# Kernel tuning notes

Measured on AMD Instinct MI355X. Metric: run time of the kernel, lower is better.

Reference implementation:

```python
import jax, jax.numpy as jnp
import numpy as np

B = 65536
N_CHILDREN = 512
HIDDEN = 64


def setup_inputs() -> dict:
    key = jax.random.key(0)
    k1, k2, k3, k4, k5, k6, k7 = jax.random.split(key, 7)
    x_cpm = jax.random.normal(k1, (B, N_CHILDREN), dtype=jnp.float32)
    x_cons = jax.random.normal(k2, (B, 1), dtype=jnp.float32)
    # per-child capacities, strictly positive (used as divisor)
    cap = jax.random.uniform(k3, (1, N_CHILDREN), dtype=jnp.float32) + 0.5
    # small MLP params (torch Linear layout: W is (out, in))
    s1 = 1.0 / np.sqrt(N_CHILDREN + 1)
    s2 = 1.0 / np.sqrt(HIDDEN)
    W1 = jax.random.normal(k4, (HIDDEN, N_CHILDREN + 1), dtype=jnp.float32) * s1
    b1 = jax.random.normal(k5, (HIDDEN,), dtype=jnp.float32) * s1
    W2 = jax.random.normal(k6, (N_CHILDREN, HIDDEN), dtype=jnp.float32) * s2
    b2 = jax.random.normal(k7, (N_CHILDREN,), dtype=jnp.float32) * s2
    return {"x_cpm": x_cpm, "x_cons": x_cons, "cap": cap,
            "W1": W1, "b1": b1, "W2": W2, "b2": b2}


def reference(x_cpm, x_cons, cap, W1, b1, W2, b2):
    cap_sum = jnp.sum(cap)  # scalar Cap_sum
    # epsilon: (B, 1) residual of the aggregate constraint
    epsilon = (x_cons * cap_sum - jnp.sum(x_cpm * cap, axis=1, keepdims=True)) / cap_sum
    concat_input = jnp.concatenate([x_cpm, epsilon], axis=1)  # (B, n_l + 1)
    h1 = jax.nn.relu(concat_input @ W1.T + b1)                # (B, 64)
    z = h1 @ W2.T + b2                                        # (B, n_l)
    # symmetric activation: tanh then row-normalize by the signed sum
    signed = jnp.tanh(z)
    h = signed / jnp.sum(signed, axis=1, keepdims=True)
    # reconcile
    x_c = (x_cpm * cap + h * epsilon * cap_sum) / cap
    return x_c
```

## Files before the change

### kernel.cpp

```cpp
#include <hip/hip_runtime.h>
#include <hip/hip_fp16.h>
#include <math.h>

#define THREADS 256
#define RPB 32
#define NBLK (65536 / RPB)

#define WS_W1    0
#define WS_W1_CH 3072
#define WS_W2    (16 * WS_W1_CH)
#define WS_W2_CH 8192
#define WS_W1L   (WS_W2 + 4 * WS_W2_CH)

#define OFF_W    0
#define SZ_W     32768
#define W1BUF_B  12288
#define OFF_H1   (OFF_W + SZ_W)
#define SZ_H1    (RPB * 68 * 4)
#define OFF_CI   (OFF_H1 + SZ_H1)
#define SZ_CI    2048
#define OFF_EPS  (OFF_CI + SZ_CI)
#define OFF_EPSC (OFF_EPS + 128)
#define SMEM_BYTES (OFF_EPSC + 128)

__device__ __forceinline__ float fast_tanh(float z) {
    float e = __expf(2.0f * z);
    return fmaf(-2.0f, __builtin_amdgcn_rcpf(e + 1.0f), 1.0f);
}

__global__ __launch_bounds__(256) void prep_kernel(
    const float* __restrict__ W1, const float* __restrict__ W2,
    float* __restrict__ ws)
{
    int tid = blockIdx.x * 256 + threadIdx.x;
    {
        int it = tid >> 11;
        int rem = tid & 2047;
        int jj = rem >> 6, c = rem & 63;
        ws[WS_W1 + it * WS_W1_CH + jj * 68 + c] = W1[c * 513 + it * 32 + jj];
    }
    {
        int j = tid & 3, kf4 = (tid >> 2) & 15, n = (tid >> 6) & 127, ch = tid >> 13;
        int swz = kf4 ^ ((9 * (n >> 2) + (n & 3)) & 15);
        ws[WS_W2 + ch * WS_W2_CH + n * 64 + swz * 4 + j] = W2[tid];
    }
    if (tid < 64) ws[WS_W1L + tid] = W1[tid * 513 + 512];
}

__global__ __launch_bounds__(THREADS, 3) void fused_rgu(
    const float* __restrict__ x, const float* __restrict__ xcons,
    const float* __restrict__ cap, const float* __restrict__ b1,
    const float* __restrict__ b2, const float* __restrict__ ws,
    float* __restrict__ out)
{
    extern __shared__ __align__(16) char smem[];
    float*          s_w    = (float*)(smem + OFF_W);
    float*          s_h1   = (float*)(smem + OFF_H1);
    float*          s_ci   = (float*)(smem + OFF_CI);
    float*          s_eps  = (float*)(smem + OFF_EPS);
    float*          s_epsC = (float*)(smem + OFF_EPSC);

    const int t    = threadIdx.x;
    const int lane = t & 63;
    const int wv   = t >> 6;
    const long r0  = (long)blockIdx.x * RPB;

    {
        const float4* src = (const float4*)(ws + WS_W1);
        float4* dst = (float4*)(smem + OFF_W);
        dst[t] = src[t]; dst[t + 256] = src[t + 256]; dst[t + 512] = src[t + 512];
    }

    float4 capA = *(const float4*)(cap + 4 * lane);
    float4 capB = *(const float4*)(cap + 256 + 4 * lane);
    {
        float c0 = cap[t], c1 = cap[t + 256];
        s_ci[t] = 1.0f / c0; s_ci[t + 256] = 1.0f / c1;
    }
    float capSum;
    {
        float p = capA.x + capA.y + capA.z + capA.w
                + capB.x + capB.y + capB.z + capB.w;
        #pragma unroll
        for (int m = 1; m < 64; m <<= 1) p += __shfl_xor(p, m, 64);
        capSum = p;
    }
    const float invCapSum = 1.0f / capSum;

    #pragma unroll
    for (int rr = 0; rr < 8; ++rr) {
        int r = wv * 8 + rr;
        const float* xr = x + (r0 + r) * 512;
        float4 xA = *(const float4*)(xr + 4 * lane);
        float4 xB = *(const float4*)(xr + 256 + 4 * lane);
        float d = fmaf(xA.x, capA.x, fmaf(xA.y, capA.y,
                  fmaf(xA.z, capA.z, fmaf(xA.w, capA.w,
                  fmaf(xB.x, capB.x, fmaf(xB.y, capB.y,
                  fmaf(xB.z, capB.z, xB.w * capB.w)))))));
        #pragma unroll
        for (int m = 1; m < 64; m <<= 1) d += __shfl_xor(d, m, 64);
        if (lane == 0) {
            float epsC = fmaf(xcons[r0 + r], capSum, -d);
            s_epsC[r] = epsC;
            s_eps[r]  = epsC * invCapSum;
        }
    }
    __syncthreads();

    const int rg = t >> 4;
    const int cg = t & 15;
    float acc0[4] = {0.f, 0.f, 0.f, 0.f};
    float acc1[4] = {0.f, 0.f, 0.f, 0.f};
    {
        const float* xg0 = x + (r0 + 2 * rg) * 512;
        const float* xg1 = xg0 + 512;
        for (int it = 0; it < 16; ++it) {
            const int b = it & 1;
            if (it < 15) {
                const float4* src = (const float4*)(ws + WS_W1 + (it + 1) * WS_W1_CH);
                float4* dst = (float4*)(smem + OFF_W + (b ^ 1) * W1BUF_B);
                dst[t] = src[t]; dst[t + 256] = src[t + 256]; dst[t + 512] = src[t + 512];
            }
            const float* w = (const float*)(smem + OFF_W + b * W1BUF_B);
            const int k0 = it * 32;
            #pragma unroll
            for (int j4 = 0; j4 < 8; ++j4) {
                float4 xv0 = *(const float4*)(xg0 + k0 + j4 * 4);
                float4 xv1 = *(const float4*)(xg1 + k0 + j4 * 4);
                const float* wb = &w[(j4 * 4) * 68 + 4 * cg];
                float wr[4][4];
                #pragma unroll
                for (int dj = 0; dj < 4; ++dj) {
                    float4 w4 = *(const float4*)(wb + dj * 68);
                    wr[dj][0] = w4.x; wr[dj][1] = w4.y; wr[dj][2] = w4.z; wr[dj][3] = w4.w;
                }
                #pragma unroll
                for (int m = 0; m < 4; ++m) {
                    acc0[m] = fmaf(xv0.x, wr[0][m], fmaf(xv0.y, wr[1][m],
                              fmaf(xv0.z, wr[2][m], fmaf(xv0.w, wr[3][m], acc0[m]))));
                    acc1[m] = fmaf(xv1.x, wr[0][m], fmaf(xv1.y, wr[1][m],
                              fmaf(xv1.z, wr[2][m], fmaf(xv1.w, wr[3][m], acc1[m]))));
                }
            }
            __syncthreads();
        }
        float4 b1v = *(const float4*)(b1 + 4 * cg);
        float4 wl  = *(const float4*)(ws + WS_W1L + 4 * cg);
        #pragma unroll
        for (int i = 0; i < 2; ++i) {
            float e = s_eps[2 * rg + i];
            const float* a = i ? acc1 : acc0;
            float4 h;
            h.x = fmaxf(a[0] + fmaf(e, wl.x, b1v.x), 0.f);
            h.y = fmaxf(a[1] + fmaf(e, wl.y, b1v.y), 0.f);
            h.z = fmaxf(a[2] + fmaf(e, wl.z, b1v.z), 0.f);
            h.w = fmaxf(a[3] + fmaf(e, wl.w, b1v.w), 0.f);
            *(float4*)&s_h1[(2 * rg + i) * 68 + 4 * cg] = h;
        }
    }

    const int ng  = t & 31;
    const int rg2 = t >> 5;
    float rsum[4] = {0.f, 0.f, 0.f, 0.f};
    unsigned tp[4][4][2];
    #pragma unroll
    for (int ch = 0; ch < 4; ++ch) {
        __syncthreads();
        {
            const float4* src = (const float4*)(ws + WS_W2 + ch * WS_W2_CH);
            float4* dst = (float4*)(smem + OFF_W);
            #pragma unroll
            for (int e8 = 0; e8 < 8; ++e8) dst[e8 * 256 + t] = src[e8 * 256 + t];
        }
        __syncthreads();
        const int n0 = ch * 128;
        float4 b2v = *(const float4*)(b2 + n0 + 4 * ng);
        float za[4][4];
        #pragma unroll
        for (int i = 0; i < 4; ++i) {
            za[i][0] = b2v.x; za[i][1] = b2v.y; za[i][2] = b2v.z; za[i][3] = b2v.w;
        }
        #pragma unroll
        for (int kf4 = 0; kf4 < 16; ++kf4) {
            float hr[4][4];
            #pragma unroll
            for (int i = 0; i < 4; ++i) {
                float4 h = *(const float4*)&s_h1[(rg2 * 4 + i) * 68 + kf4 * 4];
                hr[i][0] = h.x; hr[i][1] = h.y; hr[i][2] = h.z; hr[i][3] = h.w;
            }
            float wr2[4][4];
            #pragma unroll
            for (int m = 0; m < 4; ++m) {
                int nl = 4 * ng + m;
                int swz = kf4 ^ ((9 * ng + m) & 15);
                float4 w = *(const float4*)&s_w[nl * 64 + swz * 4];
                wr2[m][0] = w.x; wr2[m][1] = w.y; wr2[m][2] = w.z; wr2[m][3] = w.w;
            }
            #pragma unroll
            for (int i = 0; i < 4; ++i)
                #pragma unroll
                for (int m = 0; m < 4; ++m)
                    za[i][m] = fmaf(hr[i][0], wr2[m][0], fmaf(hr[i][1], wr2[m][1],
                               fmaf(hr[i][2], wr2[m][2], fmaf(hr[i][3], wr2[m][3], za[i][m]))));
        }
        #pragma unroll
        for (int i = 0; i < 4; ++i) {
            float t0 = fast_tanh(za[i][0]);
            float t1 = fast_tanh(za[i][1]);
            float t2 = fast_tanh(za[i][2]);
            float t3 = fast_tanh(za[i][3]);
            rsum[i] += (t0 + t1) + (t2 + t3);
            __half2 h01 = __floats2half2_rn(t0, t1);
            __half2 h23 = __floats2half2_rn(t2, t3);
            tp[ch][i][0] = *(unsigned*)&h01;
            tp[ch][i][1] = *(unsigned*)&h23;
        }
    }

    float rs[4];
    #pragma unroll
    for (int i = 0; i < 4; ++i) {
        float s = rsum[i];
        #pragma unroll
        for (int msk = 1; msk < 32; msk <<= 1) s += __shfl_xor(s, msk, 64);
        rs[i] = s_epsC[rg2 * 4 + i] / s;
    }

    #pragma unroll
    for (int ch = 0; ch < 4; ++ch) {
        const int c = ch * 128 + 4 * ng;
        float4 ci = *(const float4*)&s_ci[c];
        #pragma unroll
        for (int i = 0; i < 4; ++i) {
            const int r = rg2 * 4 + i;
            float4 xv = *(const float4*)(x + (r0 + r) * 512 + c);
            __half2 h01 = *(__half2*)&tp[ch][i][0];
            __half2 h23 = *(__half2*)&tp[ch][i][1];
            float2 f01 = __half22float2(h01);
            float2 f23 = __half22float2(h23);
            float ri = rs[i];
            float4 o;
            o.x = fmaf(f01.x, ri * ci.x, xv.x);
            o.y = fmaf(f01.y, ri * ci.y, xv.y);
            o.z = fmaf(f23.x, ri * ci.z, xv.z);
            o.w = fmaf(f23.y, ri * ci.w, xv.w);
            *(float4*)(out + (r0 + r) * 512 + c) = o;
        }
    }
}

extern "C" void kernel_launch(void* const* d_in, const int* in_sizes, int n_in,
                              void* d_out, int out_size, void* d_ws, size_t ws_size,
                              hipStream_t stream) {
    const float* x     = (const float*)d_in[0];
    const float* xcons = (const float*)d_in[1];
    const float* cap   = (const float*)d_in[2];
    const float* W1    = (const float*)d_in[3];
    const float* b1    = (const float*)d_in[4];
    const float* W2    = (const float*)d_in[5];
    const float* b2    = (const float*)d_in[6];
    float* out         = (float*)d_out;
    float* ws          = (float*)d_ws;

    (void)in_sizes; (void)n_in; (void)out_size; (void)ws_size;

    prep_kernel<<<128, 256, 0, stream>>>(W1, W2, ws);

    hipFuncSetAttribute((const void*)fused_rgu,
                        hipFuncAttributeMaxDynamicSharedMemorySize, SMEM_BYTES);
    fused_rgu<<<NBLK, THREADS, SMEM_BYTES, stream>>>(
        x, xcons, cap, b1, b2, ws, out);
}
```

Measured before the change: 389.3 us.

## Shrink shared-memory footprint and W2 tiles to raise occupancy to five blocks

Drops the W1 chunk padding from 3072 to 2304 floats and splits W2 into eight 64-output chunks instead of four 128-output chunks, which cuts the shared weight buffer from 32 KB to about 17 KB. The second GEMM now reuses the first GEMM's 2-row by 4-column thread mapping, and b2 is staged in shared memory. Launch bounds go from 3 to 5 blocks per SM to hide more global-memory latency. In exchange there are more W2 chunk loads and barriers, less register reuse per thread (2 rows instead of 4), and a tighter register budget.

```diff
diff --git a/kernel.cpp b/kernel.cpp
--- a/kernel.cpp
+++ b/kernel.cpp
@@ -7,19 +7,21 @@
 #define NBLK (65536 / RPB)
 
 #define WS_W1    0
-#define WS_W1_CH 3072
+#define WS_W1_CH 2304
 #define WS_W2    (16 * WS_W1_CH)
-#define WS_W2_CH 8192
-#define WS_W1L   (WS_W2 + 4 * WS_W2_CH)
+#define WS_W2_CH 4096
+#define WS_W1L   (WS_W2 + 8 * WS_W2_CH)
 
 #define OFF_W    0
-#define SZ_W     32768
-#define W1BUF_B  12288
+#define W1BUF_B  8704
+#define SZ_W     17408
 #define OFF_H1   (OFF_W + SZ_W)
 #define SZ_H1    (RPB * 68 * 4)
 #define OFF_CI   (OFF_H1 + SZ_H1)
 #define SZ_CI    2048
-#define OFF_EPS  (OFF_CI + SZ_CI)
+#define OFF_B2   (OFF_CI + SZ_CI)
+#define SZ_B2    2048
+#define OFF_EPS  (OFF_B2 + SZ_B2)
 #define OFF_EPSC (OFF_EPS + 128)
 #define SMEM_BYTES (OFF_EPSC + 128)
 
@@ -40,14 +42,14 @@
         ws[WS_W1 + it * WS_W1_CH + jj * 68 + c] = W1[c * 513 + it * 32 + jj];
     }
     {
-        int j = tid & 3, kf4 = (tid >> 2) & 15, n = (tid >> 6) & 127, ch = tid >> 13;
+        int j = tid & 3, kf4 = (tid >> 2) & 15, n = (tid >> 6) & 63, ch = tid >> 12;
         int swz = kf4 ^ ((9 * (n >> 2) + (n & 3)) & 15);
         ws[WS_W2 + ch * WS_W2_CH + n * 64 + swz * 4 + j] = W2[tid];
     }
     if (tid < 64) ws[WS_W1L + tid] = W1[tid * 513 + 512];
 }
 
-__global__ __launch_bounds__(THREADS, 3) void fused_rgu(
+__global__ __launch_bounds__(THREADS, 5) void fused_rgu(
     const float* __restrict__ x, const float* __restrict__ xcons,
     const float* __restrict__ cap, const float* __restrict__ b1,
     const float* __restrict__ b2, const float* __restrict__ ws,
@@ -57,6 +59,7 @@
     float*          s_w    = (float*)(smem + OFF_W);
     float*          s_h1   = (float*)(smem + OFF_H1);
     float*          s_ci   = (float*)(smem + OFF_CI);
+    float*          s_b2   = (float*)(smem + OFF_B2);
     float*          s_eps  = (float*)(smem + OFF_EPS);
     float*          s_epsC = (float*)(smem + OFF_EPSC);
 
@@ -68,7 +71,8 @@
     {
         const float4* src = (const float4*)(ws + WS_W1);
         float4* dst = (float4*)(smem + OFF_W);
-        dst[t] = src[t]; dst[t + 256] = src[t + 256]; dst[t + 512] = src[t + 512];
+        dst[t] = src[t]; dst[t + 256] = src[t + 256];
+        if (t < 32) dst[t + 512] = src[t + 512];
     }
 
     float4 capA = *(const float4*)(cap + 4 * lane);
@@ -76,6 +80,7 @@
     {
         float c0 = cap[t], c1 = cap[t + 256];
         s_ci[t] = 1.0f / c0; s_ci[t + 256] = 1.0f / c1;
+        s_b2[t] = b2[t];     s_b2[t + 256] = b2[t + 256];
     }
     float capSum;
     {
@@ -119,7 +124,8 @@
             if (it < 15) {
                 const float4* src = (const float4*)(ws + WS_W1 + (it + 1) * WS_W1_CH);
                 float4* dst = (float4*)(smem + OFF_W + (b ^ 1) * W1BUF_B);
-                dst[t] = src[t]; dst[t + 256] = src[t + 256]; dst[t + 512] = src[t + 512];
+                dst[t] = src[t]; dst[t + 256] = src[t + 256];
+                if (t < 32) dst[t + 512] = src[t + 512];
             }
             const float* w = (const float*)(smem + OFF_W + b * W1BUF_B);
             const int k0 = it * 32;
@@ -159,52 +165,50 @@
         }
     }
 
-    const int ng  = t & 31;
-    const int rg2 = t >> 5;
-    float rsum[4] = {0.f, 0.f, 0.f, 0.f};
-    unsigned tp[4][4][2];
-    #pragma unroll
-    for (int ch = 0; ch < 4; ++ch) {
+    float rsum[2] = {0.f, 0.f};
+    unsigned tp[8][2][2];
+    #pragma unroll
+    for (int ch = 0; ch < 8; ++ch) {
         __syncthreads();
         {
             const float4* src = (const float4*)(ws + WS_W2 + ch * WS_W2_CH);
             float4* dst = (float4*)(smem + OFF_W);
             #pragma unroll
-            for (int e8 = 0; e8 < 8; ++e8) dst[e8 * 256 + t] = src[e8 * 256 + t];
+            for (int e4 = 0; e4 < 4; ++e4) dst[e4 * 256 + t] = src[e4 * 256 + t];
         }
         __syncthreads();
-        const int n0 = ch * 128;
-        float4 b2v = *(const float4*)(b2 + n0 + 4 * ng);
-        float za[4][4];
-        #pragma unroll
-        for (int i = 0; i < 4; ++i) {
+        const int n0 = ch * 64;
+        float4 b2v = *(const float4*)&s_b2[n0 + 4 * cg];
+        float za[2][4];
+        #pragma unroll
+        for (int i = 0; i < 2; ++i) {
             za[i][0] = b2v.x; za[i][1] = b2v.y; za[i][2] = b2v.z; za[i][3] = b2v.w;
         }
         #pragma unroll
         for (int kf4 = 0; kf4 < 16; ++kf4) {
-            float hr[4][4];
-            #pragma unroll
-            for (int i = 0; i < 4; ++i) {
-                float4 h = *(const float4*)&s_h1[(rg2 * 4 + i) * 68 + kf4 * 4];
+            float hr[2][4];
+            #pragma unroll
+            for (int i = 0; i < 2; ++i) {
+                float4 h = *(const float4*)&s_h1[(2 * rg + i) * 68 + kf4 * 4];
                 hr[i][0] = h.x; hr[i][1] = h.y; hr[i][2] = h.z; hr[i][3] = h.w;
             }
             float wr2[4][4];
             #pragma unroll
             for (int m = 0; m < 4; ++m) {
-                int nl = 4 * ng + m;
-                int swz = kf4 ^ ((9 * ng + m) & 15);
+                int nl = 4 * cg + m;
+                int swz = kf4 ^ ((9 * cg + m) & 15);
                 float4 w = *(const float4*)&s_w[nl * 64 + swz * 4];
                 wr2[m][0] = w.x; wr2[m][1] = w.y; wr2[m][2] = w.z; wr2[m][3] = w.w;
             }
             #pragma unroll
-            for (int i = 0; i < 4; ++i)
+            for (int i = 0; i < 2; ++i)
                 #pragma unroll
                 for (int m = 0; m < 4; ++m)
                     za[i][m] = fmaf(hr[i][0], wr2[m][0], fmaf(hr[i][1], wr2[m][1],
                                fmaf(hr[i][2], wr2[m][2], fmaf(hr[i][3], wr2[m][3], za[i][m]))));
         }
         #pragma unroll
-        for (int i = 0; i < 4; ++i) {
+        for (int i = 0; i < 2; ++i) {
             float t0 = fast_tanh(za[i][0]);
             float t1 = fast_tanh(za[i][1]);
             float t2 = fast_tanh(za[i][2]);
@@ -217,22 +221,22 @@
         }
     }
 
-    float rs[4];
-    #pragma unroll
-    for (int i = 0; i < 4; ++i) {
+    float rs[2];
+    #pragma unroll
+    for (int i = 0; i < 2; ++i) {
         float s = rsum[i];
         #pragma unroll
-        for (int msk = 1; msk < 32; msk <<= 1) s += __shfl_xor(s, msk, 64);
-        rs[i] = s_epsC[rg2 * 4 + i] / s;
-    }
-
-    #pragma unroll
-    for (int ch = 0; ch < 4; ++ch) {
-        const int c = ch * 128 + 4 * ng;
+        for (int msk = 1; msk < 16; msk <<= 1) s += __shfl_xor(s, msk, 64);
+        rs[i] = s_epsC[2 * rg + i] / s;
+    }
+
+    #pragma unroll
+    for (int ch = 0; ch < 8; ++ch) {
+        const int c = ch * 64 + 4 * cg;
         float4 ci = *(const float4*)&s_ci[c];
         #pragma unroll
-        for (int i = 0; i < 4; ++i) {
-            const int r = rg2 * 4 + i;
+        for (int i = 0; i < 2; ++i) {
+            const int r = 2 * rg + i;
             float4 xv = *(const float4*)(x + (r0 + r) * 512 + c);
             __half2 h01 = *(__half2*)&tp[ch][i][0];
             __half2 h23 = *(__half2*)&tp[ch][i][1];
```

After: 509.3 us. 30.8% more time.

## Retile first GEMM to 4 rows x 2 cols per thread with swizzled packed W1

Applied to the files above, without the earlier changes.

Changes the first-layer GEMM mapping from 2 rows x 4 hidden units per thread to 4 rows x 2 hidden units. W1 is repacked in the prep kernel into an XOR-swizzled, pair-interleaved layout without padding, so each W1 stage is smaller and loads as two float4s per k-group. The aim is fewer LDS reads per FMA and a smaller staging buffer, but each thread now issues more global x loads per step. b2 is staged in shared memory, and launch bounds drop from 3 to 2 blocks per CU, which gives the compiler more registers at the cost of occupancy.

```diff
diff --git a/kernel.cpp b/kernel.cpp
--- a/kernel.cpp
+++ b/kernel.cpp
@@ -7,19 +7,21 @@
 #define NBLK (65536 / RPB)
 
 #define WS_W1    0
-#define WS_W1_CH 3072
+#define WS_W1_CH 2048
 #define WS_W2    (16 * WS_W1_CH)
 #define WS_W2_CH 8192
 #define WS_W1L   (WS_W2 + 4 * WS_W2_CH)
 
 #define OFF_W    0
+#define W1BUF_B  8192
 #define SZ_W     32768
-#define W1BUF_B  12288
 #define OFF_H1   (OFF_W + SZ_W)
 #define SZ_H1    (RPB * 68 * 4)
 #define OFF_CI   (OFF_H1 + SZ_H1)
 #define SZ_CI    2048
-#define OFF_EPS  (OFF_CI + SZ_CI)
+#define OFF_B2   (OFF_CI + SZ_CI)
+#define SZ_B2    2048
+#define OFF_EPS  (OFF_B2 + SZ_B2)
 #define OFF_EPSC (OFF_EPS + 128)
 #define SMEM_BYTES (OFF_EPSC + 128)
 
@@ -36,8 +38,12 @@
     {
         int it = tid >> 11;
         int rem = tid & 2047;
-        int jj = rem >> 6, c = rem & 63;
-        ws[WS_W1 + it * WS_W1_CH + jj * 68 + c] = W1[c * 513 + it * 32 + jj];
+        int j  = rem & 1;
+        int kb = (rem >> 1) & 1;
+        int m  = (rem >> 2) & 15;
+        int p  = rem >> 6;
+        int off = it * WS_W1_CH + p * 64 + ((m ^ (p & 15)) << 2) + kb * 2 + j;
+        ws[WS_W1 + off] = W1[(2 * p + j) * 513 + it * 32 + 2 * m + kb];
     }
     {
         int j = tid & 3, kf4 = (tid >> 2) & 15, n = (tid >> 6) & 127, ch = tid >> 13;
@@ -47,7 +53,7 @@
     if (tid < 64) ws[WS_W1L + tid] = W1[tid * 513 + 512];
 }
 
-__global__ __launch_bounds__(THREADS, 3) void fused_rgu(
+__global__ __launch_bounds__(THREADS, 2) void fused_rgu(
     const float* __restrict__ x, const float* __restrict__ xcons,
     const float* __restrict__ cap, const float* __restrict__ b1,
     const float* __restrict__ b2, const float* __restrict__ ws,
@@ -57,6 +63,7 @@
     float*          s_w    = (float*)(smem + OFF_W);
     float*          s_h1   = (float*)(smem + OFF_H1);
     float*          s_ci   = (float*)(smem + OFF_CI);
+    float*          s_b2   = (float*)(smem + OFF_B2);
     float*          s_eps  = (float*)(smem + OFF_EPS);
     float*          s_epsC = (float*)(smem + OFF_EPSC);
 
@@ -68,7 +75,7 @@
     {
         const float4* src = (const float4*)(ws + WS_W1);
         float4* dst = (float4*)(smem + OFF_W);
-        dst[t] = src[t]; dst[t + 256] = src[t + 256]; dst[t + 512] = src[t + 512];
+        dst[t] = src[t]; dst[t + 256] = src[t + 256];
     }
 
     float4 capA = *(const float4*)(cap + 4 * lane);
@@ -76,6 +83,7 @@
     {
         float c0 = cap[t], c1 = cap[t + 256];
         s_ci[t] = 1.0f / c0; s_ci[t + 256] = 1.0f / c1;
+        s_b2[t] = b2[t];     s_b2[t + 256] = b2[t + 256];
     }
     float capSum;
     {
@@ -107,55 +115,52 @@
     }
     __syncthreads();
 
-    const int rg = t >> 4;
-    const int cg = t & 15;
-    float acc0[4] = {0.f, 0.f, 0.f, 0.f};
-    float acc1[4] = {0.f, 0.f, 0.f, 0.f};
-    {
-        const float* xg0 = x + (r0 + 2 * rg) * 512;
+    const int rg = t >> 5;
+    const int cg = t & 31;
+    float acc[4][2] = {{0.f,0.f},{0.f,0.f},{0.f,0.f},{0.f,0.f}};
+    {
+        const float* xg0 = x + (r0 + 4 * rg) * 512;
         const float* xg1 = xg0 + 512;
+        const float* xg2 = xg0 + 1024;
+        const float* xg3 = xg0 + 1536;
+        const int pswz = (cg & 15);
         for (int it = 0; it < 16; ++it) {
             const int b = it & 1;
             if (it < 15) {
                 const float4* src = (const float4*)(ws + WS_W1 + (it + 1) * WS_W1_CH);
                 float4* dst = (float4*)(smem + OFF_W + (b ^ 1) * W1BUF_B);
-                dst[t] = src[t]; dst[t + 256] = src[t + 256]; dst[t + 512] = src[t + 512];
-            }
-            const float* w = (const float*)(smem + OFF_W + b * W1BUF_B);
+                dst[t] = src[t]; dst[t + 256] = src[t + 256];
+            }
+            const float* wp = (const float*)(smem + OFF_W + b * W1BUF_B) + cg * 64;
             const int k0 = it * 32;
             #pragma unroll
             for (int j4 = 0; j4 < 8; ++j4) {
                 float4 xv0 = *(const float4*)(xg0 + k0 + j4 * 4);
                 float4 xv1 = *(const float4*)(xg1 + k0 + j4 * 4);
-                const float* wb = &w[(j4 * 4) * 68 + 4 * cg];
-                float wr[4][4];
+                float4 xv2 = *(const float4*)(xg2 + k0 + j4 * 4);
+                float4 xv3 = *(const float4*)(xg3 + k0 + j4 * 4);
+                float4 w0 = *(const float4*)&wp[((2 * j4)     ^ pswz) << 2];
+                float4 w1 = *(const float4*)&wp[((2 * j4 + 1) ^ pswz) << 2];
                 #pragma unroll
-                for (int dj = 0; dj < 4; ++dj) {
-                    float4 w4 = *(const float4*)(wb + dj * 68);
-                    wr[dj][0] = w4.x; wr[dj][1] = w4.y; wr[dj][2] = w4.z; wr[dj][3] = w4.w;
+                for (int i = 0; i < 4; ++i) {
+                    float4 xv = (i == 0) ? xv0 : (i == 1) ? xv1 : (i == 2) ? xv2 : xv3;
+                    acc[i][0] = fmaf(xv.x, w0.x, fmaf(xv.y, w0.z,
+                                fmaf(xv.z, w1.x, fmaf(xv.w, w1.z, acc[i][0]))));
+                    acc[i][1] = fmaf(xv.x, w0.y, fmaf(xv.y, w0.w,
+                                fmaf(xv.z, w1.y, fmaf(xv.w, w1.w, acc[i][1]))));
                 }
-                #pragma unroll
-                for (int m = 0; m < 4; ++m) {
-                    acc0[m] = fmaf(xv0.x, wr[0][m], fmaf(xv0.y, wr[1][m],
-                              fmaf(xv0.z, wr[2][m], fmaf(xv0.w, wr[3][m], acc0[m]))));
-                    acc1[m] = fmaf(xv1.x, wr[0][m], fmaf(xv1.y, wr[1][m],
-                              fmaf(xv1.z, wr[2][m], fmaf(xv1.w, wr[3][m], acc1[m]))));
-                }
             }
             __syncthreads();
         }
-        float4 b1v = *(const float4*)(b1 + 4 * cg);
-        float4 wl  = *(const float4*)(ws + WS_W1L + 4 * cg);
-        #pragma unroll
-        for (int i = 0; i < 2; ++i) {
-            float e = s_eps[2 * rg + i];
-            const float* a = i ? acc1 : acc0;
-            float4 h;
-            h.x = fmaxf(a[0] + fmaf(e, wl.x, b1v.x), 0.f);
-            h.y = fmaxf(a[1] + fmaf(e, wl.y, b1v.y), 0.f);
-            h.z = fmaxf(a[2] + fmaf(e, wl.z, b1v.z), 0.f);
-            h.w = fmaxf(a[3] + fmaf(e, wl.w, b1v.w), 0.f);
-            *(float4*)&s_h1[(2 * rg + i) * 68 + 4 * cg] = h;
+        float2 b1v = *(const float2*)(b1 + 2 * cg);
+        float2 wl  = *(const float2*)(ws + WS_W1L + 2 * cg);
+        #pragma unroll
+        for (int i = 0; i < 4; ++i) {
+            float e = s_eps[4 * rg + i];
+            float2 h;
+            h.x = fmaxf(acc[i][0] + fmaf(e, wl.x, b1v.x), 0.f);
+            h.y = fmaxf(acc[i][1] + fmaf(e, wl.y, b1v.y), 0.f);
+            *(float2*)&s_h1[(4 * rg + i) * 68 + 2 * cg] = h;
         }
     }
 
@@ -174,7 +179,7 @@
         }
         __syncthreads();
         const int n0 = ch * 128;
-        float4 b2v = *(const float4*)(b2 + n0 + 4 * ng);
+        float4 b2v = *(const float4*)&s_b2[n0 + 4 * ng];
         float za[4][4];
         #pragma unroll
         for (int i = 0; i < 4; ++i) {
```

New measurement: 451.9 us. 1.16x slower.
